# Optimization experiments

Measured on AMD Instinct MI355X. Metric: run time of the kernel, lower is better.

## Reference

```python
import jax, jax.numpy as jnp
import numpy as np

SIGMA = 2.0
KSIZE = int(SIGMA * 6 + 1)  # 13, already odd


def _gauss(x, mu, sigma):
    return 1.0 / (sigma * (2.0 * np.pi) ** 0.5) * np.exp(-((x - mu) ** 2) / (2.0 * sigma ** 2))


def _gaussian_kernel_3d(ksize, sigma):
    l = ksize // 2
    c = np.arange(-l, l + 1, dtype=np.float32)
    g = _gauss(c, 0.0, sigma).astype(np.float32)  # [K]
    # dense separable outer product, same as torch module's triple loop
    w = g[:, None, None] * g[None, :, None] * g[None, None, :]  # [K,K,K]
    return jnp.asarray(w)[None, None]  # [O=1, I=1, K, K, K]


def setup_inputs() -> dict:
    key = jax.random.key(0)
    x = jax.random.normal(key, (2, 1, 192, 192, 192), dtype=jnp.float32)
    W = _gaussian_kernel_3d(KSIZE, SIGMA)
    return {"x": x, "W": W}


def reference(x, W):
    pad = KSIZE // 2
    return jax.lax.conv_general_dilated(
        x, W,
        window_strides=(1, 1, 1),
        padding=[(pad, pad), (pad, pad), (pad, pad)],
        dimension_numbers=("NCDHW", "OIDHW", "NCDHW"),
        feature_group_count=1,
    )
```

## Files before the change

kernel.cpp:

```cpp
#include <hip/hip_runtime.h>
#include <hip/hip_bf16.h>
#include <hip/hip_fp16.h>


#define DIM 192
#define DIM2 (192 * 192)
#define NIMG 2
#define TOTAL (NIMG * DIM * DIM2)
#define NQ (TOTAL / 4)
#define NPAIR (NQ / 2)

typedef float f32x4 __attribute__((ext_vector_type(4)));

#define GTAPS                                                     \
    constexpr float G[13] = {                                     \
        2.2159242e-03f, 8.7641505e-03f, 2.6995483e-02f,           \
        6.4758800e-02f, 1.2098536e-01f, 1.7603266e-01f,           \
        1.9947114e-01f, 1.7603266e-01f, 1.2098536e-01f,           \
        6.4758800e-02f, 2.6995483e-02f, 8.7641505e-03f,           \
        2.2159242e-03f };

__device__ __forceinline__ float4 ld_h4(const uint2* __restrict__ p) {
    uint2 u = *p;
    __half2 h0 = *(__half2*)&u.x;
    __half2 h1 = *(__half2*)&u.y;
    return make_float4(__low2float(h0), __high2float(h0),
                       __low2float(h1), __high2float(h1));
}
__device__ __forceinline__ uint2 st_h4(float4 v) {
    __half2 h0 = __floats2half2_rn(v.x, v.y);
    __half2 h1 = __floats2half2_rn(v.z, v.w);
    uint2 u;
    u.x = *(unsigned*)&h0;
    u.y = *(unsigned*)&h1;
    return u;
}

__global__ __launch_bounds__(256) void blur_w(const float4* __restrict__ in,
                                              uint4* __restrict__ out) {
    GTAPS
    const int j = blockIdx.x * 256 + threadIdx.x;
    const int jp = j % 24;
    const int rowq = (j / 24) * 48;

    float f[24];
#pragma unroll
    for (int d = 0; d < 6; ++d) {
        int qq = 2 * jp - 2 + d;
        const float m = (qq >= 0 && qq < 48) ? 1.0f : 0.0f;
        qq = min(max(qq, 0), 47);
        float4 v = in[rowq + qq];
        if (d < 2 || d > 3) {
            v.x *= m; v.y *= m; v.z *= m; v.w *= m;
        }
        *(float4*)&f[d * 4] = v;
    }

    float o[8];
#pragma unroll
    for (int t = 0; t < 8; ++t) {
        float a = 0.0f;
#pragma unroll
        for (int k = 0; k < 13; ++k) a += G[k] * f[t + 2 + k];
        o[t] = a;
    }
    uint2 lo = st_h4(make_float4(o[0], o[1], o[2], o[3]));
    uint2 hi = st_h4(make_float4(o[4], o[5], o[6], o[7]));
    uint4 r; r.x = lo.x; r.y = lo.y; r.z = hi.x; r.w = hi.y;
    out[j] = r;
}

#define CH 12
#define NSTEP (CH + 12)
#define NCHUNK (DIM / CH)

template <int S, bool OUT_F32, int CLIP>
__device__ __forceinline__ void col_body(const uint2* __restrict__ in,
                                         void* __restrict__ out_,
                                         int base, int d0) {
    GTAPS
    float4 v[NSTEP];
#pragma unroll
    for (int s = 0; s < NSTEP; ++s) {
        bool valid = true;
        if (CLIP < 0) valid = (s >= 6);
        if (CLIP > 0) valid = (s < NSTEP - 6);
        if (valid) v[s] = ld_h4(&in[base + (d0 - 6 + s) * S]);
        else       v[s] = make_float4(0.f, 0.f, 0.f, 0.f);
    }
#pragma unroll
    for (int t = 0; t < CH; ++t) {
        float4 a = make_float4(0.f, 0.f, 0.f, 0.f);
#pragma unroll
        for (int k = 0; k < 13; ++k) {
            const float g = G[k];
            a.x += g * v[t + k].x;
            a.y += g * v[t + k].y;
            a.z += g * v[t + k].z;
            a.w += g * v[t + k].w;
        }
        const int o = base + (d0 + t) * S;
        if (OUT_F32) {
            f32x4 av;
            av.x = a.x; av.y = a.y; av.z = a.z; av.w = a.w;
            __builtin_nontemporal_store(av, &((f32x4*)out_)[o]);
        } else {
            ((uint2*)out_)[o] = st_h4(a);
        }
    }
}

template <int Q, int M, int S, bool OUT_F32>
__global__ __launch_bounds__(128) void col_blur(const uint2* __restrict__ in,
                                                void* __restrict__ out_) {
    const int gt = blockIdx.x * 128 + threadIdx.x;
    const int chunk = gt / 18432;
    const int c = gt % 18432;
    const int base = (c / Q) * M + (c % Q);
    const int d0 = chunk * CH;

    if (chunk == 0)                col_body<S, OUT_F32, -1>(in, out_, base, d0);
    else if (chunk == NCHUNK - 1)  col_body<S, OUT_F32, +1>(in, out_, base, d0);
    else                           col_body<S, OUT_F32,  0>(in, out_, base, d0);
}

extern "C" void kernel_launch(void* const* d_in, const int* in_sizes, int n_in,
                              void* d_out, int out_size, void* d_ws, size_t ws_size,
                              hipStream_t stream) {
    const float* x = (const float*)d_in[0];
    float* out = (float*)d_out;
    uint2* tmp1 = (uint2*)d_ws;
    uint2* tmp2 = ((uint2*)d_ws) + NQ;

    blur_w<<<NPAIR / 256, 256, 0, stream>>>((const float4*)x, (uint4*)tmp1);
    col_blur<48, 9216, 48, false><<<2304, 128, 0, stream>>>(tmp1, (void*)tmp2);
    col_blur<9216, 1769472, 9216, true><<<2304, 128, 0, stream>>>(tmp2, (void*)out);
}
```

Baseline: 42.53 us.

## Fuse H and D blur passes into one tiled kernel via shared memory

```diff
diff --git a/kernel.cpp b/kernel.cpp
--- a/kernel.cpp
+++ b/kernel.cpp
@@ -20,7 +20,7 @@
         6.4758800e-02f, 2.6995483e-02f, 8.7641505e-03f,           \
         2.2159242e-03f };
 
-__device__ __forceinline__ float4 ld_h4(const uint2* __restrict__ p) {
+__device__ __forceinline__ float4 ld_h4(const uint2* p) {
     uint2 u = *p;
     __half2 h0 = *(__half2*)&u.x;
     __half2 h1 = *(__half2*)&u.y;
@@ -70,58 +70,90 @@
     out[j] = r;
 }
 
-#define CH 12
-#define NSTEP (CH + 12)
-#define NCHUNK (DIM / CH)
+#define YO 16
+#define ZO 20
+#define ZS 32
+#define YPAD 17
 
-template <int S, bool OUT_F32, int CLIP>
-__device__ __forceinline__ void col_body(const uint2* __restrict__ in,
-                                         void* __restrict__ out_,
-                                         int base, int d0) {
+__global__ __launch_bounds__(256) void col_hd(const uint2* __restrict__ tmp1,
+                                              float* __restrict__ out) {
     GTAPS
-    float4 v[NSTEP];
+    __shared__ uint2 h[ZS][8][YPAD];
+
+    const int b = blockIdx.x;
+    const int xg = b % 6;
+    const int yt = (b / 6) % 12;
+    const int zt = (b / 72) % 10;
+    const int img = b / 720;
+    const int y0 = yt * YO;
+    const int z0 = zt * ZO;
+    const int t = threadIdx.x;
+
+    {
+        const int zs = t >> 3;
+        const int xq = t & 7;
+        const int iz = z0 - 6 + zs;
+        const float zm = (iz >= 0 && iz < DIM) ? 1.0f : 0.0f;
+        const int izc = min(max(iz, 0), DIM - 1);
+        const int x = xg * 8 + xq;
+        const uint2* __restrict__ col =
+            tmp1 + (size_t)(img * DIM + izc) * DIM * 48 + x;
+
+        float4 v[28];
 #pragma unroll
-    for (int s = 0; s < NSTEP; ++s) {
-        bool valid = true;
-        if (CLIP < 0) valid = (s >= 6);
-        if (CLIP > 0) valid = (s < NSTEP - 6);
-        if (valid) v[s] = ld_h4(&in[base + (d0 - 6 + s) * S]);
-        else       v[s] = make_float4(0.f, 0.f, 0.f, 0.f);
-    }
+        for (int s = 0; s < 28; ++s) {
+            const int iy = y0 - 6 + s;
+            const float ym = (iy >= 0 && iy < DIM) ? 1.0f : 0.0f;
+            const int iyc = min(max(iy, 0), DIM - 1);
+            float4 vv = ld_h4(&col[iyc * 48]);
+            vv.x *= ym; vv.y *= ym; vv.z *= ym; vv.w *= ym;
+            v[s] = vv;
+        }
 #pragma unroll
-    for (int t = 0; t < CH; ++t) {
-        float4 a = make_float4(0.f, 0.f, 0.f, 0.f);
+        for (int yy = 0; yy < YO; ++yy) {
+            float4 a = make_float4(0.f, 0.f, 0.f, 0.f);
 #pragma unroll
-        for (int k = 0; k < 13; ++k) {
-            const float g = G[k];
-            a.x += g * v[t + k].x;
-            a.y += g * v[t + k].y;
-            a.z += g * v[t + k].z;
-            a.w += g * v[t + k].w;
-        }
-        const int o = base + (d0 + t) * S;
-        if (OUT_F32) {
-            f32x4 av;
-            av.x = a.x; av.y = a.y; av.z = a.z; av.w = a.w;
-            __builtin_nontemporal_store(av, &((f32x4*)out_)[o]);
-        } else {
-            ((uint2*)out_)[o] = st_h4(a);
+            for (int k = 0; k < 13; ++k) {
+                const float g = G[k];
+                a.x += g * v[yy + k].x;
+                a.y += g * v[yy + k].y;
+                a.z += g * v[yy + k].z;
+                a.w += g * v[yy + k].w;
+            }
+            a.x *= zm; a.y *= zm; a.z *= zm; a.w *= zm;
+            h[zs][xq][yy] = st_h4(a);
         }
     }
-}
+    __syncthreads();
 
-template <int Q, int M, int S, bool OUT_F32>
-__global__ __launch_bounds__(128) void col_blur(const uint2* __restrict__ in,
-                                                void* __restrict__ out_) {
-    const int gt = blockIdx.x * 128 + threadIdx.x;
-    const int chunk = gt / 18432;
-    const int c = gt % 18432;
-    const int base = (c / Q) * M + (c % Q);
-    const int d0 = chunk * CH;
+    {
+        const int xq = t & 7;
+        const int zh = (t >> 3) & 1;
+        const int y = t >> 4;
+        const int x = xg * 8 + xq;
 
-    if (chunk == 0)                col_body<S, OUT_F32, -1>(in, out_, base, d0);
-    else if (chunk == NCHUNK - 1)  col_body<S, OUT_F32, +1>(in, out_, base, d0);
-    else                           col_body<S, OUT_F32,  0>(in, out_, base, d0);
+#pragma unroll
+        for (int zi = 0; zi < 10; ++zi) {
+            const int z = zh * 10 + zi;
+            if (z0 + z < DIM) {
+                float4 a = make_float4(0.f, 0.f, 0.f, 0.f);
+#pragma unroll
+                for (int k = 0; k < 13; ++k) {
+                    const float g = G[k];
+                    float4 hv = ld_h4(&h[z + k][xq][y]);
+                    a.x += g * hv.x;
+                    a.y += g * hv.y;
+                    a.z += g * hv.z;
+                    a.w += g * hv.w;
+                }
+                const size_t o =
+                    ((size_t)(img * DIM + z0 + z) * DIM + (y0 + y)) * 48 + x;
+                f32x4 av;
+                av.x = a.x; av.y = a.y; av.z = a.z; av.w = a.w;
+                __builtin_nontemporal_store(av, &((f32x4*)out)[o]);
+            }
+        }
+    }
 }
 
 extern "C" void kernel_launch(void* const* d_in, const int* in_sizes, int n_in,
@@ -130,9 +162,7 @@
     const float* x = (const float*)d_in[0];
     float* out = (float*)d_out;
     uint2* tmp1 = (uint2*)d_ws;
-    uint2* tmp2 = ((uint2*)d_ws) + NQ;
 
     blur_w<<<NPAIR / 256, 256, 0, stream>>>((const float4*)x, (uint4*)tmp1);
-    col_blur<48, 9216, 48, false><<<2304, 128, 0, stream>>>(tmp1, (void*)tmp2);
-    col_blur<9216, 1769472, 9216, true><<<2304, 128, 0, stream>>>(tmp2, (void*)out);
+    col_hd<<<1440, 256, 0, stream>>>(tmp1, out);
 }
```

New measurement: 46.40 us. 9.1% more time.
